# Kernel optimization log

Measured on AMD Instinct MI355X. Metric: run time of the kernel, lower is better.

## Reference

```python
import jax, jax.numpy as jnp
import numpy as np

NUM_SELECT = 300
OUT_H = 448
OUT_W = 448


def setup_inputs() -> dict:
    key = jax.random.key(0)
    k1, k2, k3 = jax.random.split(key, 3)
    B, Q, C = 4, 900, 91
    pred_logits = jax.random.normal(k1, (B, Q, C), dtype=jnp.float32)
    pred_boxes = jax.random.uniform(k2, (B, Q, 4), dtype=jnp.float32)  # cxcywh in [0,1)
    pred_masks = jax.random.normal(k3, (B, Q, 28, 28), dtype=jnp.float32)
    # all images same size so resize output shape is static under jit
    target_sizes = jnp.full((B, 2), OUT_H, dtype=jnp.int64 if jax.config.jax_enable_x64 else jnp.int32)
    return {"pred_logits": pred_logits, "pred_boxes": pred_boxes,
            "pred_masks": pred_masks, "target_sizes": target_sizes}


def _box_cxcywh_to_xyxy(b):
    cx, cy, w, h = jnp.split(b, 4, axis=-1)
    return jnp.concatenate([cx - 0.5 * w, cy - 0.5 * h, cx + 0.5 * w, cy + 0.5 * h], axis=-1)


def reference(pred_logits, pred_boxes, pred_masks, target_sizes):
    B, Q, C = pred_logits.shape
    # sigmoid + topk over flattened (query, class) axis
    prob = jax.nn.sigmoid(pred_logits).reshape(B, Q * C)
    scores, topk_idx = jax.lax.top_k(prob, NUM_SELECT)          # [B, K]
    topk_boxes = topk_idx // C                                   # query index [B, K]
    labels = topk_idx % C                                        # class index [B, K]

    boxes = _box_cxcywh_to_xyxy(pred_boxes)                      # [B, Q, 4]
    boxes = jnp.take_along_axis(boxes, topk_boxes[:, :, None], axis=1)  # [B, K, 4]

    img_h = target_sizes[:, 0].astype(boxes.dtype)
    img_w = target_sizes[:, 1].astype(boxes.dtype)
    scale = jnp.stack([img_w, img_h, img_w, img_h], axis=1)      # [B, 4]
    boxes = boxes * scale[:, None, :]

    # gather top-k masks: [B, K, 28, 28]
    masks = jnp.take_along_axis(pred_masks, topk_boxes[:, :, None, None], axis=1)
    masks = masks.astype(jnp.float16)
    # bilinear, half-pixel centers == torch align_corners=False
    resize_one = lambda m: jax.image.resize(m, (NUM_SELECT, OUT_H, OUT_W), method="bilinear")
    masks = jax.vmap(resize_one)(masks)                          # [B, K, OUT_H, OUT_W] fp16

    return scores, labels, boxes, masks
```

## Files before the change

### kernel.cpp

```cpp
#include <hip/hip_runtime.h>
#include <hip/hip_fp16.h>

#define QN 900
#define CN 91
#define TOTN (QN * CN)
#define KSEL 300
#define BN 4
#define OUTW 448
#define MASKPIX (OUTW * OUTW)
#define OFFS_LABELS (BN * KSEL)
#define OFFS_BOXES  (2 * BN * KSEL)
#define OFFS_MASKS  (6 * BN * KSEL)
#define MAXC 2048
#define BT 1024

typedef float floatx4 __attribute__((ext_vector_type(4)));

static __device__ __forceinline__ unsigned fkey(float f) {
    unsigned u = __float_as_uint(f);
    return (u & 0x80000000u) ? ~u : (u | 0x80000000u);
}

__global__ __launch_bounds__(BT) void select_kernel(
    const float* __restrict__ logits, const float* __restrict__ boxes,
    const int* __restrict__ tsz, float* out, int* qsel)
{
    const int b = blockIdx.x;
    const int tid = threadIdx.x;
    const int lane = tid & 63;
    const float* lg = logits + (size_t)b * TOTN;

    __shared__ unsigned hlane[256 * 33];
    __shared__ unsigned hist[256];
    __shared__ int sh_bin, sh_want, sh_chunk;
    __shared__ unsigned sh_above, sh_cnt;
    __shared__ int cidx[MAXC];
    __shared__ unsigned ckey[MAXC];

    for (int i = tid; i < 256 * 33; i += BT) hlane[i] = 0;
    __syncthreads();
    {
        const int sl = lane & 31;
        for (int i = tid; i < TOTN; i += BT) {
            unsigned key = fkey(lg[i]);
            atomicAdd(&hlane[(key >> 24) * 33 + sl], 1u);
        }
    }
    __syncthreads();
    if (tid < 256) {
        unsigned s = 0;
#pragma unroll
        for (int l = 0; l < 32; ++l) s += hlane[tid * 33 + l];
        hist[tid] = s;
    }
    __syncthreads();

    unsigned prefix = 0;
    int want = KSEL;
#pragma unroll
    for (int round = 0; round < 2; ++round) {
        const int shift = 24 - 8 * round;
        if (round > 0) {
            if (tid < 256) hist[tid] = 0;
            __syncthreads();
            for (int i = tid; i < TOTN; i += BT) {
                unsigned key = fkey(lg[i]);
                if ((key & 0xFF000000u) == prefix)
                    atomicAdd(&hist[(key >> 16) & 255u], 1u);
            }
            __syncthreads();
        }
        if (tid < 64) {
            unsigned p = hist[tid * 4] + hist[tid * 4 + 1]
                       + hist[tid * 4 + 2] + hist[tid * 4 + 3];
            unsigned suffix = p;
#pragma unroll
            for (int o = 1; o < 64; o <<= 1) {
                unsigned t = __shfl_down(suffix, o);
                if (tid + o < 64) suffix += t;
            }
            unsigned nxt = __shfl_down(suffix, 1);
            if (tid == 63) nxt = 0;
            bool flag = (suffix >= (unsigned)want) && (nxt < (unsigned)want);
            if (flag) { sh_chunk = tid; sh_above = nxt; }
        }
        __syncthreads();
        if (tid == 0) {
            int ch = sh_chunk;
            unsigned acc = sh_above;
            int j = 3;
            for (; j > 0; --j) {
                if (acc + hist[ch * 4 + j] >= (unsigned)want) break;
                acc += hist[ch * 4 + j];
            }
            sh_bin = ch * 4 + j;
            sh_want = want - (int)acc;
        }
        __syncthreads();
        prefix |= ((unsigned)sh_bin << shift);
        want = sh_want;
        __syncthreads();
    }
    const unsigned T16 = prefix >> 16;

    if (tid == 0) sh_cnt = 0;
    __syncthreads();
    for (int i = tid; i < TOTN; i += BT) {
        unsigned key = fkey(lg[i]);
        if ((key >> 16) >= T16) {
            unsigned p = atomicAdd(&sh_cnt, 1u);
            if (p < MAXC) { cidx[p] = i; ckey[p] = key; }
        }
    }
    __syncthreads();
    const int ncand = min((int)sh_cnt, MAXC);

    const float fh = (float)tsz[b * 2 + 0];
    const float fw = (float)tsz[b * 2 + 1];

    for (int c = tid; c < ncand; c += BT) {
        const unsigned kc = ckey[c];
        const int ic = cidx[c];
        int rank = 0;
        for (int s = 0; s < ncand; ++s) {
            unsigned ks = ckey[s];
            if (ks > kc || (ks == kc && cidx[s] < ic)) ++rank;
        }
        if (rank < KSEL) {
            float lf = lg[ic];
            float score = 1.0f / (1.0f + expf(-lf));
            int q = ic / CN;
            int label = ic - q * CN;

            out[b * KSEL + rank] = score;
            out[OFFS_LABELS + b * KSEL + rank] = (float)label;

            const float* bx = boxes + ((size_t)b * QN + q) * 4;
            float cx = bx[0], cy = bx[1], ww = bx[2], hh = bx[3];
            float* ob = out + OFFS_BOXES + ((size_t)(b * KSEL + rank)) * 4;
            ob[0] = (cx - 0.5f * ww) * fw;
            ob[1] = (cy - 0.5f * hh) * fh;
            ob[2] = (cx + 0.5f * ww) * fw;
            ob[3] = (cy + 0.5f * hh) * fh;

            qsel[b * KSEL + rank] = q;
        }
    }
}

#define SPLIT 4
#define ROWSB (OUTW / SPLIT)

__global__ __launch_bounds__(256) void mask_kernel(
    const float* __restrict__ masks, const int* __restrict__ qsel,
    float* __restrict__ out)
{
    const int mk = blockIdx.x >> 2;
    const int part = blockIdx.x & 3;
    const int b = mk / KSEL;
    const int q = qsel[mk];
    const float* __restrict__ src = masks + ((size_t)b * QN + q) * 784;

    const int j = threadIdx.x & 127;
    const int rhalf = threadIdx.x >> 7;
    if (j >= 112) return;

    const int qd = j & 3;
    const int i4 = j >> 2;
    const int c0 = i4 - 1 + (qd >> 1);
    const int c0c = c0 < 0 ? 0 : c0;
    const int c1c = (c0 + 1 > 27) ? 27 : c0 + 1;
    const float toff = 0.25f * (float)qd - ((qd >= 2) ? 1.0f : 0.0f);
    const float t0 = 0.53125f + toff, t1 = 0.59375f + toff,
                t2 = 0.65625f + toff, t3 = 0.71875f + toff;

    const int ybase = part * ROWSB + rhalf;
    float* optr = out + OFFS_MASKS + (size_t)mk * MASKPIX
                + (size_t)ybase * OUTW + j * 4;

    float sy = (float)ybase * 0.0625f - 0.46875f;
    for (int k = 0; k < ROWSB / 2; ++k) {
        float yf = floorf(sy);
        float ty = sy - yf;
        int iy = (int)yf;
        int y0 = iy < 0 ? 0 : iy;
        int y1 = (iy + 1 > 27) ? 27 : iy + 1;
        const float* r0 = src + y0 * 28;
        const float* r1 = src + y1 * 28;
        float m00 = r0[c0c], m01 = r0[c1c];
        float m10 = r1[c0c], m11 = r1[c1c];
        float v0 = fmaf(ty, m10 - m00, m00);
        float v1 = fmaf(ty, m11 - m01, m01);
        float dv = v1 - v0;
        floatx4 w;
        w.x = fmaf(t0, dv, v0);
        w.y = fmaf(t1, dv, v0);
        w.z = fmaf(t2, dv, v0);
        w.w = fmaf(t3, dv, v0);
        *reinterpret_cast<floatx4*>(optr) = w;
        optr += 2 * OUTW;
        sy += 0.125f;
    }
}

extern "C" void kernel_launch(void* const* d_in, const int* in_sizes, int n_in,
                              void* d_out, int out_size, void* d_ws, size_t ws_size,
                              hipStream_t stream) {
    const float* pred_logits = (const float*)d_in[0];
    const float* pred_boxes  = (const float*)d_in[1];
    const float* pred_masks  = (const float*)d_in[2];
    const int*   target_sz   = (const int*)d_in[3];
    float* out = (float*)d_out;
    int* qsel = (int*)d_ws;

    select_kernel<<<BN, BT, 0, stream>>>(pred_logits, pred_boxes, target_sz, out, qsel);
    mask_kernel<<<BN * KSEL * SPLIT, 256, 0, stream>>>(pred_masks, qsel, out);
}
```

Measured before the change: 272.6 us.

## Flatten mask resize into persistent grid-stride loop over all output float4s

Replaces the per-mask, per-row-split grid (4800 blocks with 16 idle lanes of 128) with 256 persistent blocks that each walk a contiguous range of float4 output elements. Every thread computes its mask, row and column from a flat index, so all lanes stay busy and consecutive threads write consecutive memory. In exchange each element now pays for integer divisions, a qsel lookup and recomputed column weights instead of reusing per-thread constants across rows, and only 256 blocks may be too few to saturate the device's write bandwidth.

Result: slower. 438.1 us (+60.7%).

```diff
diff --git a/kernel.cpp b/kernel.cpp
--- a/kernel.cpp
+++ b/kernel.cpp
@@ -13,6 +13,10 @@
 #define OFFS_MASKS  (6 * BN * KSEL)
 #define MAXC 2048
 #define BT 1024
+
+#define MBLOCKS 256
+#define F4PB 235200u
+#define MITERS 919
 
 typedef float floatx4 __attribute__((ext_vector_type(4)));
 
@@ -148,38 +152,32 @@
     }
 }
 
-#define SPLIT 4
-#define ROWSB (OUTW / SPLIT)
-
 __global__ __launch_bounds__(256) void mask_kernel(
     const float* __restrict__ masks, const int* __restrict__ qsel,
     float* __restrict__ out)
 {
-    const int mk = blockIdx.x >> 2;
-    const int part = blockIdx.x & 3;
-    const int b = mk / KSEL;
-    const int q = qsel[mk];
-    const float* __restrict__ src = masks + ((size_t)b * QN + q) * 784;
-
-    const int j = threadIdx.x & 127;
-    const int rhalf = threadIdx.x >> 7;
-    if (j >= 112) return;
-
-    const int qd = j & 3;
-    const int i4 = j >> 2;
-    const int c0 = i4 - 1 + (qd >> 1);
-    const int c0c = c0 < 0 ? 0 : c0;
-    const int c1c = (c0 + 1 > 27) ? 27 : c0 + 1;
-    const float toff = 0.25f * (float)qd - ((qd >= 2) ? 1.0f : 0.0f);
-    const float t0 = 0.53125f + toff, t1 = 0.59375f + toff,
-                t2 = 0.65625f + toff, t3 = 0.71875f + toff;
-
-    const int ybase = part * ROWSB + rhalf;
-    float* optr = out + OFFS_MASKS + (size_t)mk * MASKPIX
-                + (size_t)ybase * OUTW + j * 4;
-
-    float sy = (float)ybase * 0.0625f - 0.46875f;
-    for (int k = 0; k < ROWSB / 2; ++k) {
+    unsigned g = blockIdx.x * F4PB + threadIdx.x;
+    const unsigned gend = (blockIdx.x + 1) * F4PB;
+    float* omask = out + OFFS_MASKS;
+
+    for (int it = 0; it < MITERS; ++it, g += 256) {
+        if (g >= gend) break;
+        unsigned grow = g / 112u;
+        int j = (int)(g - grow * 112u);
+        unsigned mk = grow / 448u;
+        int y = (int)(grow - mk * 448u);
+        int b = (int)(mk / (unsigned)KSEL);
+        int q = qsel[mk];
+        const float* __restrict__ src = masks + ((size_t)b * QN + q) * 784;
+
+        int qd = j & 3;
+        int i4 = j >> 2;
+        int c0 = i4 - 1 + (qd >> 1);
+        int c0c = c0 < 0 ? 0 : c0;
+        int c1c = (c0 + 1 > 27) ? 27 : c0 + 1;
+        float toff = 0.25f * (float)qd - ((qd >= 2) ? 1.0f : 0.0f);
+
+        float sy = (float)y * 0.0625f - 0.46875f;
         float yf = floorf(sy);
         float ty = sy - yf;
         int iy = (int)yf;
@@ -193,13 +191,11 @@
         float v1 = fmaf(ty, m11 - m01, m01);
         float dv = v1 - v0;
         floatx4 w;
-        w.x = fmaf(t0, dv, v0);
-        w.y = fmaf(t1, dv, v0);
-        w.z = fmaf(t2, dv, v0);
-        w.w = fmaf(t3, dv, v0);
-        *reinterpret_cast<floatx4*>(optr) = w;
-        optr += 2 * OUTW;
-        sy += 0.125f;
+        w.x = fmaf(0.53125f + toff, dv, v0);
+        w.y = fmaf(0.59375f + toff, dv, v0);
+        w.z = fmaf(0.65625f + toff, dv, v0);
+        w.w = fmaf(0.71875f + toff, dv, v0);
+        *reinterpret_cast<floatx4*>(omask + (size_t)g * 4) = w;
     }
 }
 
@@ -214,5 +210,5 @@
     int* qsel = (int*)d_ws;
 
     select_kernel<<<BN, BT, 0, stream>>>(pred_logits, pred_boxes, target_sz, out, qsel);
-    mask_kernel<<<BN * KSEL * SPLIT, 256, 0, stream>>>(pred_masks, qsel, out);
-}
+    mask_kernel<<<MBLOCKS, 256, 0, stream>>>(pred_masks, qsel, out);
+}
```
